# Optimization experiments

Hardware: AMD Instinct MI355X
Metric: run time of the kernel (lower is better)

The kernel has to match this reference:

```python
import jax, jax.numpy as jnp
import numpy as np

MULT = 0.001      # DEFAULT_MULTIPLIER
N_ITERS = 9       # self.N
N_K = 4           # self.l
BINARY = ('mul', 'add')  # original binary_ops_list order


def _valid_pairs(nc, r, lc):
    # replicate flag logic over (i, j) candidate pairs
    nri = N_ITERS - r
    out = []
    for i in range(nc - 1):
        for j in range(i + 1, nc):
            if nri == lc - 1:
                flag = i >= 3
            elif nri == lc:
                flag = j >= 3
            else:
                flag = nri > lc
            if flag:
                out.append((i, j))
    return out


def _act(name, res):
    if name == 'sigmoid':
        return MULT * jax.nn.sigmoid(res)
    if name == 'tanh':
        return MULT * jnp.tanh(res)
    if name == 'minus':
        return 1.0 - res
    return res  # identity


def run_cell(x, h_prev, L, R, b, w, plan=None):
    """Faithful RRNNforGRUCell tree-structure search.
    record mode (plan=None): data-dependent decisions taken concretely (eager).
    replay mode (plan given): purely differentiable jnp replay of recorded plan.
    """
    record = plan is None
    if record:
        plan = []
    xv = x.reshape(-1)
    hv = h_prev.reshape(-1)
    H = xv.shape[0]
    zero = jnp.zeros((H,), dtype=xv.dtype)
    G = []            # max_vector per iteration
    second = []       # second-ranked vector per iteration
    comp_src = []     # G-indices backing current components_list
    for r in range(N_ITERS):
        cand = [xv, hv, zero] + [G[g] for g in comp_src]
        nc = len(cand)
        C = jnp.stack(cand)                       # (nc, H)
        CL = jnp.einsum('ch,khd->ckd', C, L)      # (nc, 4, H) all s_i @ L_k
        CR = jnp.einsum('ch,khd->ckd', C, R)      # (nc, 4, H) all s_j @ R_k
        V = []
        if record:
            entries = []
            for (i, j) in _valid_pairs(nc, r, len(comp_src)):
                for k in range(N_K):
                    for bf in BINARY:
                        if bf == 'mul':
                            res = CL[i, k] * CR[j, k] + b[k]
                        else:
                            res = CL[i, k] + CR[j, k] + b[k]
                        if float(jnp.max(jnp.abs(res))) >= 1.0:
                            acts = ('sigmoid', 'tanh')
                        else:
                            acts = ('sigmoid', 'tanh', 'minus', 'identity')
                        for a in acts:
                            V.append(_act(a, res))
                            entries.append((i, j, k, bf, a))
        else:
            entries = plan[r]['entries']
            cache = {}
            for (i, j, k, bf, a) in entries:
                key = (i, j, k, bf)
                if key not in cache:
                    if bf == 'mul':
                        cache[key] = CL[i, k] * CR[j, k] + b[k]
                    else:
                        cache[key] = CL[i, k] + CR[j, k] + b[k]
                V.append(_act(a, cache[key]))
        Vs = jnp.stack(V)          # (nV, H)
        scores = Vs @ w            # (nV,) scoring Linear(H,1,bias=False)
        if record:
            s = np.asarray(scores)
            max_idx = int(np.argmax(s))
            # position of the element ranked second-smallest (original code)
            second_idx = int(np.where(np.argsort(s) == 1)[0][0])
            plan.append({'entries': entries, 'max_idx': max_idx, 'second_idx': second_idx})
        else:
            max_idx = plan[r]['max_idx']
            second_idx = plan[r]['second_idx']
        probs = jax.nn.softmax(scores)
        # NOTE: replicates original bug: loop uses stale `i` == nc-2, so every
        # v is weighted by probabilities[nc-2].
        max_vec = probs[nc - 2] * Vs.sum(axis=0)
        second.append(V[second_idx])
        G.append(max_vec)
        i, j = entries[max_idx][0], entries[max_idx][1]
        if i > 2 and j > 2:
            comp_src[i - 3] = r
            del comp_src[j - 3]
        elif i <= 2 and j > 2:
            comp_src[j - 3] = r
        else:
            comp_src.append(r)
    Gs = jnp.stack(G)                       # (9, H)
    out = (Gs[-1], Gs, Gs @ w, jnp.stack(second) @ w)
    return (out, plan) if record else out


def setup_inputs() -> dict:
    key = jax.random.key(0)
    ks = jax.random.split(key, 6)
    H = 2048
    return {
        'x': jax.random.normal(ks[0], (1, H), jnp.float32),
        'h_prev': jax.random.normal(ks[1], (1, H), jnp.float32),
        'L': MULT * jax.random.normal(ks[2], (N_K, H, H), jnp.float32),
        'R': MULT * jax.random.normal(ks[3], (N_K, H, H), jnp.float32),
        'b': MULT * jax.random.normal(ks[4], (N_K, H), jnp.float32),
        'w': jax.random.normal(ks[5], (H,), jnp.float32),
    }


def reference(x, h_prev, L, R, b, w):
    # returns (h_next, G_stack [9,H], scores of G [9], second_scores [9])
    out, _ = run_cell(x, h_prev, L, R, b, w)
    return out
```

## Files before the change

### kernel.cpp

```cpp
#include <hip/hip_runtime.h>
#include <math.h>

#define HDIM 2048
#define NK 4
#define NIT 9
#define NSID 11
#define MAXPAIRS 36
#define MAXBASES (MAXPAIRS*8)
#define NACC 16
#define NBS (MAXBASES + NACC)

#define CACHE_SZ (NSID*2*NK*HDIM)
#define OFF_CACHE 0
#define OFF_AMAX   (OFF_CACHE + CACHE_SZ)
#define OFF_DOTR_D (OFF_AMAX + MAXBASES)
#define OFF_DOTS_D (OFF_DOTR_D + 2*MAXBASES)
#define OFF_DOTT_D (OFF_DOTS_D + 2*MAXBASES)
#define PLAN_SZ 152
#define OFF_PLAN0 (OFF_DOTT_D + 2*MAXBASES)
#define OFF_PLAN1 (OFF_PLAN0 + PLAN_SZ)
#define OFF_STATE (OFF_PLAN1 + PLAN_SZ)
#define OFF_SUMW_D (OFF_STATE + 16)
#define OFF_GT8   (OFF_SUMW_D + 16)
#define OFF_PART  (OFF_GT8 + 8*HDIM)

__device__ __forceinline__ float wredmax(float v){
#pragma unroll
  for(int o=32;o;o>>=1) v = fmaxf(v,__shfl_down(v,o,64));
  return v;
}
__device__ __forceinline__ float wredsum(float v){
#pragma unroll
  for(int o=32;o;o>>=1) v += __shfl_down(v,o,64);
  return v;
}
__device__ __forceinline__ double wredsumd(double v){
#pragma unroll
  for(int o=32;o;o>>=1) v += __shfl_down(v,o,64);
  return v;
}

__device__ void build_plan(int r, int lc, const int* cs, int* plan){
  int nc = 3 + lc;
  int nri = NIT - r;
  int np = 0;
  for(int i=0;i<nc-1;i++){
    for(int j=i+1;j<nc;j++){
      bool flag;
      if (nri == lc-1)      flag = (i>=3);
      else if (nri == lc)   flag = (j>=3);
      else                  flag = (nri > lc);
      if(flag){
        plan[8+np]            = i;
        plan[8+MAXPAIRS+np]   = j;
        plan[8+2*MAXPAIRS+np] = (i<3)? i : 3+cs[i-3];
        plan[8+3*MAXPAIRS+np] = (j<3)? j : 3+cs[j-3];
        np++;
      }
    }
  }
  plan[0]=nc; plan[1]=np; plan[2]=np*8;
}

__global__ __launch_bounds__(256) void kvecmat(const float* __restrict__ va,
                                               const float* __restrict__ vb,
                                               const float* __restrict__ w,
                                               const float* __restrict__ L,
                                               const float* __restrict__ R,
                                               float* __restrict__ ws,
                                               int nvec){
  int bid = blockIdx.x;
  int tid = threadIdx.x;
  int nmain = nvec << 8;
  if (bid >= nmain){
    int ib = bid - nmain;
    for(int i = ib*256+tid; i < 8*HDIM; i += 32*256)
      ws[OFF_CACHE + 16*HDIM + i] = 0.f;
    if (ib == 0){
      double s = 0.0;
      for(int d=tid; d<HDIM; d+=256) s += (double)w[d];
      s = wredsumd(s);
      __shared__ double red[4];
      int wv = tid>>6, ln = tid&63;
      if(!ln) red[wv]=s;
      __syncthreads();
      if(tid==0){
        *(double*)(ws + OFF_SUMW_D) = red[0]+red[1]+red[2]+red[3];
        int* st = (int*)(ws + OFF_STATE);
        for(int q=0;q<=8;q++) st[q]=0;
        build_plan(0, 0, st+1, (int*)(ws + OFF_PLAN0));
      }
    }
    return;
  }
  int vec   = bid >> 8;
  int b     = bid & 255;
  int combo = b >> 5;
  int hc    = b & 31;
  const float* v = vec ? vb : va;
  __shared__ float vs[64];
  if (tid < 64) vs[tid] = v[hc*64 + tid];
  __syncthreads();
  int m = combo>>2, k = combo&3;
  const float* M = (m==0?L:R) + (size_t)k*HDIM*HDIM + (size_t)hc*64*HDIM + tid*4;
  float ax0=0.f, ay0=0.f, az0=0.f, aw0=0.f;
  float ax1=0.f, ay1=0.f, az1=0.f, aw1=0.f;
#pragma unroll 8
  for(int h=0; h<64; h++){
    const float4 f0 = *reinterpret_cast<const float4*>(M + (size_t)h*HDIM);
    const float4 f1 = *reinterpret_cast<const float4*>(M + (size_t)h*HDIM + 1024);
    float vv = vs[h];
    ax0 = fmaf(vv, f0.x, ax0); ay0 = fmaf(vv, f0.y, ay0);
    az0 = fmaf(vv, f0.z, az0); aw0 = fmaf(vv, f0.w, aw0);
    ax1 = fmaf(vv, f1.x, ax1); ay1 = fmaf(vv, f1.y, ay1);
    az1 = fmaf(vv, f1.z, az1); aw1 = fmaf(vv, f1.w, aw1);
  }
  float* P = ws + OFF_PART + ((size_t)(vec*8+combo)*32 + hc)*HDIM + tid*4;
  float4 o0; o0.x=ax0; o0.y=ay0; o0.z=az0; o0.w=aw0;
  float4 o1; o1.x=ax1; o1.y=ay1; o1.z=az1; o1.w=aw1;
  *reinterpret_cast<float4*>(P) = o0;
  *reinterpret_cast<float4*>(P + 1024) = o1;
}

__global__ __launch_bounds__(256) void kreduce(float* __restrict__ ws, int sid0){
  int b = blockIdx.x;
  int vec = b>>6, rem = b&63;
  int combo = rem>>3, dc8 = rem&7;
  int d = dc8*256 + threadIdx.x;
  const float* p = ws + OFF_PART + (size_t)(vec*8+combo)*32*HDIM + d;
  float s = 0.f;
#pragma unroll
  for(int hc=0; hc<32; hc++) s += p[(size_t)hc*HDIM];
  int m = combo>>2, k = combo&3;
  int sid = sid0 + vec;
  ws[OFF_CACHE + ((size_t)(sid*2+m)*NK + k)*HDIM + d] = s;
}

__global__ __launch_bounds__(256) void kbaseaccum(const float* __restrict__ bvec,
                                                  const float* __restrict__ w,
                                                  float* __restrict__ ws, int par){
  const int* plan = (const int*)(ws + (par ? OFF_PLAN1 : OFF_PLAN0));
  int nb = plan[2];
  int tid = threadIdx.x;
  if (blockIdx.x < MAXBASES){
    int t = blockIdx.x;
    if (t >= nb) return;
    int p = t>>3, k=(t>>1)&3, bf=t&1;
    int si = plan[8+2*MAXPAIRS+p], sj = plan[8+3*MAXPAIRS+p];
    const float* CL = ws + OFF_CACHE + ((size_t)(si*2+0)*NK + k)*HDIM;
    const float* CR = ws + OFF_CACHE + ((size_t)(sj*2+1)*NK + k)*HDIM;
    const float* bk = bvec + (size_t)k*HDIM;
    int d0 = tid*8;
    float am=0.f; double dr=0.0, ds=0.0, dt=0.0;
#pragma unroll
    for(int half=0; half<2; half++){
      int d = d0 + half*4;
      const float4 a4 = *reinterpret_cast<const float4*>(CL + d);
      const float4 c4 = *reinterpret_cast<const float4*>(CR + d);
      const float4 b4 = *reinterpret_cast<const float4*>(bk + d);
      const float4 w4 = *reinterpret_cast<const float4*>(w  + d);
      float av[4]={a4.x,a4.y,a4.z,a4.w};
      float cv[4]={c4.x,c4.y,c4.z,c4.w};
      float bv[4]={b4.x,b4.y,b4.z,b4.w};
      float wv4[4]={w4.x,w4.y,w4.z,w4.w};
#pragma unroll
      for(int q=0;q<4;q++){
        float res = (bf==0) ? __fadd_rn(__fmul_rn(av[q],cv[q]), bv[q])
                            : __fadd_rn(__fadd_rn(av[q],cv[q]), bv[q]);
        float wd = wv4[q];
        am = fmaxf(am, fabsf(res));
        float sg = 1.0f/(1.0f+expf(-res));
        float th = tanhf(res);
        dr += (double)res*(double)wd;
        ds += (double)sg *(double)wd;
        dt += (double)th *(double)wd;
      }
    }
    am = wredmax(am); dr = wredsumd(dr); ds = wredsumd(ds); dt = wredsumd(dt);
    __shared__ double redd[4][3];
    __shared__ float  redm[4];
    int wv = tid>>6, ln = tid&63;
    if(!ln){ redm[wv]=am; redd[wv][0]=dr; redd[wv][1]=ds; redd[wv][2]=dt; }
    __syncthreads();
    if(!tid){
      float A=redm[0]; double Dr=redd[0][0], Ds=redd[0][1], Dt=redd[0][2];
      for(int q=1;q<4;q++){ A=fmaxf(A,redm[q]); Dr+=redd[q][0]; Ds+=redd[q][1]; Dt+=redd[q][2]; }
      ws[OFF_AMAX+t]=A;
      ((double*)(ws+OFF_DOTR_D))[t]=Dr;
      ((double*)(ws+OFF_DOTS_D))[t]=Ds;
      ((double*)(ws+OFF_DOTT_D))[t]=Dt;
    }
  } else {
    int bid2 = blockIdx.x - MAXBASES;
    int bc = bid2 >> 1;
    int dh = bid2 & 1;
    int d = dh*1024 + tid*4;
    float acc[4] = {0.f,0.f,0.f,0.f};
    for(int t=bc; t<nb; t+=8){
      int p=t>>3, k=(t>>1)&3, bf=t&1;
      int si = plan[8+2*MAXPAIRS+p], sj = plan[8+3*MAXPAIRS+p];
      const float4 a4 = *reinterpret_cast<const float4*>(ws + OFF_CACHE + ((size_t)(si*2+0)*NK+k)*HDIM + d);
      const float4 c4 = *reinterpret_cast<const float4*>(ws + OFF_CACHE + ((size_t)(sj*2+1)*NK+k)*HDIM + d);
      const float4 b4 = *reinterpret_cast<const float4*>(bvec + (size_t)k*HDIM + d);
      float av[4]={a4.x,a4.y,a4.z,a4.w};
      float cv[4]={c4.x,c4.y,c4.z,c4.w};
      float bv[4]={b4.x,b4.y,b4.z,b4.w};
#pragma unroll
      for(int q=0;q<4;q++){
        float res = (bf==0) ? (av[q]*cv[q] + bv[q]) : (av[q] + cv[q] + bv[q]);
        float ex  = __expf(-res);
        float sig = 1.0f/(1.0f+ex);
        float ex2 = ex*ex;
        float th  = (1.0f-ex2)/(1.0f+ex2);
        acc[q] += sig + th;
      }
    }
    float4 o; o.x=acc[0]; o.y=acc[1]; o.z=acc[2]; o.w=acc[3];
    *reinterpret_cast<float4*>(ws + OFF_GT8 + (size_t)bc*HDIM + d) = o;
  }
}

__global__ __launch_bounds__(256) void kselfin(const float* __restrict__ w,
                                               float* __restrict__ ws,
                                               float* __restrict__ out, int r){
  __shared__ double s4[MAXBASES][4];
  __shared__ int    sna[MAXBASES];
  __shared__ double tval[256];
  __shared__ int    tidx[256];
  __shared__ double tz[256];
  __shared__ int    tcnt[256];
  __shared__ double sh_smax;
  __shared__ float  sh_psel;
  __shared__ int    sh_c4;
  int par = r & 1;
  int* plan = (int*)(ws + (par ? OFF_PLAN1 : OFF_PLAN0));
  int nc = plan[0];
  int nb = plan[2];
  double sumw = *(const double*)(ws + OFF_SUMW_D);
  const double* DR = (const double*)(ws+OFF_DOTR_D);
  const double* DS = (const double*)(ws+OFF_DOTS_D);
  const double* DT = (const double*)(ws+OFF_DOTT_D);
  int tid = threadIdx.x;
  for(int t=tid; t<nb; t+=256){
    float A  = ws[OFF_AMAX+t];
    double Dr = DR[t], Ds = DS[t], Dt = DT[t];
    sna[t] = (A < 1.0f) ? 4 : 2;
    s4[t][0] = 0.001*Ds;
    s4[t][1] = 0.001*Dt;
    s4[t][2] = sumw - Dr;
    s4[t][3] = Dr;
  }
  __syncthreads();
  double best = -1e300; int bidx = 1<<30;
  for(int q=tid; q<nb*4; q+=256){
    int t=q>>2, a=q&3;
    if (a < sna[t]){
      double v = s4[t][a];
      if (v > best || (v==best && q < bidx)){ best=v; bidx=q; }
    }
  }
  tval[tid]=best; tidx[tid]=bidx;
  __syncthreads();
  if (tid==0){
    double bb=tval[0]; int bi=tidx[0];
    for(int u=1;u<256;u++)
      if (tval[u] > bb || (tval[u]==bb && tidx[u] < bi)){ bb=tval[u]; bi=tidx[u]; }
    sh_smax = bb;
    tidx[0] = bi;
  }
  __syncthreads();
  double smax = sh_smax;
  double s1 = s4[0][1];
  double z = 0.0; int cnt = 0;
  for(int q=tid; q<nb*4; q+=256){
    int t=q>>2, a=q&3;
    if (a < sna[t]){
      double v = s4[t][a];
      z += exp(v - smax);
      cnt += (v < s1) ? 1 : 0;
    }
  }
  tz[tid]=z; tcnt[tid]=cnt;
  __syncthreads();
  if (tid==0){
    int bi = tidx[0];
    double Z=0.0; int rank=0;
    for(int u=0;u<256;u++){ Z += tz[u]; rank += tcnt[u]; }
    int need = nc-2, e=0; double s_sel=0.0;
    for(int t=0;t<nb;t++){
      int n = sna[t];
      if (need < e+n){ s_sel = s4[t][need-e]; break; }
      e += n;
    }
    double psel = exp(s_sel - smax) / Z;
    int e2=0; double ssec=0.0;
    for(int t=0;t<nb;t++){
      int n = sna[t];
      if (rank < e2+n){ ssec = s4[t][rank-e2]; break; }
      e2 += n;
    }
    out[10*HDIM + 9 + r] = (float)ssec;
    int c4=0;
    for(int t=0;t<nb;t++) c4 += (sna[t]==4) ? 1 : 0;
    int mt = bi>>2;
    int mp = mt>>3;
    int ci = plan[8+mp], cj = plan[8+MAXPAIRS+mp];
    sh_psel = (float)psel;
    sh_c4   = c4;
    int* st = (int*)(ws + OFF_STATE);
    int lc = st[0];
    int* cs = st+1;
    if (ci>2 && cj>2){
      cs[ci-3] = r;
      for(int q2=cj-3; q2<lc-1; q2++) cs[q2]=cs[q2+1];
      lc--;
    } else if (ci<=2 && cj>2){
      cs[cj-3] = r;
    } else {
      cs[lc] = r; lc++;
    }
    st[0]=lc;
    if (r+1 < NIT)
      build_plan(r+1, lc, cs, (int*)(ws + ((par^1) ? OFF_PLAN1 : OFF_PLAN0)));
  }
  __syncthreads();
  float psel = sh_psel;
  float c4f  = (float)sh_c4;
  float dot = 0.f;
#pragma unroll
  for(int q=0;q<8;q++){
    int d = q*256 + tid;
    float s = 0.f;
#pragma unroll
    for(int bc=0; bc<8; bc++) s += ws[OFF_GT8 + (size_t)bc*HDIM + d];
    float g = psel * (0.001f*s + c4f);
    out[HDIM + (size_t)r*HDIM + d] = g;
    if (r == NIT-1) out[d] = g;
    dot = fmaf(g, w[d], dot);
  }
  dot = wredsum(dot);
  __shared__ float redf[4];
  int wv = tid>>6, ln = tid&63;
  if(!ln) redf[wv]=dot;
  __syncthreads();
  if(!tid) out[10*HDIM + r] = redf[0]+redf[1]+redf[2]+redf[3];
}

extern "C" void kernel_launch(void* const* d_in, const int* in_sizes, int n_in,
                              void* d_out, int out_size, void* d_ws, size_t ws_size,
                              hipStream_t stream){
  const float* x = (const float*)d_in[0];
  const float* h = (const float*)d_in[1];
  const float* L = (const float*)d_in[2];
  const float* R = (const float*)d_in[3];
  const float* b = (const float*)d_in[4];
  const float* w = (const float*)d_in[5];
  float* out = (float*)d_out;
  float* ws  = (float*)d_ws;

  kvecmat<<<512+32,256,0,stream>>>(x, h, w, L, R, ws, 2);
  kreduce<<<128,256,0,stream>>>(ws, 0);
  for(int r=0;r<NIT;r++){
    if (r > 0){
      kvecmat<<<256,256,0,stream>>>(out + HDIM + (size_t)(r-1)*HDIM, nullptr, w, L, R, ws, 1);
      kreduce<<<64,256,0,stream>>>(ws, 3+(r-1));
    }
    kbaseaccum<<<NBS,256,0,stream>>>(b, w, ws, r&1);
    kselfin<<<1,256,0,stream>>>(w, ws, out, r);
  }
}
```

Measured before the change: 546.0 us.

## Stream matrix tiles through triple-buffered LDS with async global_load_lds

Replaces direct per-thread float4 global loads of the L/R tile rows with asynchronous global-to-LDS copies into a three-stage ring buffer. Explicit vmcnt waits and barriers let later tiles load while the current one is consumed from LDS. The aim is more bytes in flight and better overlap for this bandwidth-bound matrix-vector stage. The cost is 48KB of LDS per block, which may reduce occupancy, plus extra barriers and hand-tuned wait counts that must match the number of outstanding loads.

```diff
diff --git a/kernel.cpp b/kernel.cpp
--- a/kernel.cpp
+++ b/kernel.cpp
@@ -99,22 +99,52 @@
   int hc    = b & 31;
   const float* v = vec ? vb : va;
   __shared__ float vs[64];
+  __shared__ __align__(16) float lbuf[3][2*HDIM];
   if (tid < 64) vs[tid] = v[hc*64 + tid];
   __syncthreads();
   int m = combo>>2, k = combo&3;
-  const float* M = (m==0?L:R) + (size_t)k*HDIM*HDIM + (size_t)hc*64*HDIM + tid*4;
+  const float* tile = (m==0?L:R) + (size_t)k*HDIM*HDIM + (size_t)hc*64*HDIM;
+  int wv = tid >> 6, ln = tid & 63;
+
+#define STAGEC(g, bi) do{ \
+    const float* s_ = tile + (size_t)(g)*2*HDIM + (size_t)(wv*4)*256 + ln*4; \
+    _Pragma("unroll") \
+    for(int i_=0;i_<4;i_++){ \
+      __builtin_amdgcn_global_load_lds( \
+        (const __attribute__((address_space(1))) void*)(s_ + i_*256), \
+        (__attribute__((address_space(3))) void*)(&lbuf[bi][(wv*4+i_)*256]), \
+        16, 0, 0); \
+    } \
+  }while(0)
+
   float ax0=0.f, ay0=0.f, az0=0.f, aw0=0.f;
   float ax1=0.f, ay1=0.f, az1=0.f, aw1=0.f;
-#pragma unroll 8
-  for(int h=0; h<64; h++){
-    const float4 f0 = *reinterpret_cast<const float4*>(M + (size_t)h*HDIM);
-    const float4 f1 = *reinterpret_cast<const float4*>(M + (size_t)h*HDIM + 1024);
-    float vv = vs[h];
-    ax0 = fmaf(vv, f0.x, ax0); ay0 = fmaf(vv, f0.y, ay0);
-    az0 = fmaf(vv, f0.z, az0); aw0 = fmaf(vv, f0.w, aw0);
-    ax1 = fmaf(vv, f1.x, ax1); ay1 = fmaf(vv, f1.y, ay1);
-    az1 = fmaf(vv, f1.z, az1); aw1 = fmaf(vv, f1.w, aw1);
-  }
+  STAGEC(0,0);
+  STAGEC(1,1);
+  STAGEC(2,2);
+#pragma unroll
+  for(int g=0; g<32; g++){
+    int bi = g % 3;
+    if (g <= 29)      asm volatile("s_waitcnt vmcnt(8)" ::: "memory");
+    else if (g == 30) asm volatile("s_waitcnt vmcnt(4)" ::: "memory");
+    else              asm volatile("s_waitcnt vmcnt(0)" ::: "memory");
+    __builtin_amdgcn_s_barrier();
+    __builtin_amdgcn_sched_barrier(0);
+#pragma unroll
+    for(int rr=0; rr<2; rr++){
+      float vv = vs[g*2+rr];
+      const float4 f0 = *reinterpret_cast<const float4*>(&lbuf[bi][rr*HDIM + tid*4]);
+      const float4 f1 = *reinterpret_cast<const float4*>(&lbuf[bi][rr*HDIM + 1024 + tid*4]);
+      ax0 = fmaf(vv, f0.x, ax0); ay0 = fmaf(vv, f0.y, ay0);
+      az0 = fmaf(vv, f0.z, az0); aw0 = fmaf(vv, f0.w, aw0);
+      ax1 = fmaf(vv, f1.x, ax1); ay1 = fmaf(vv, f1.y, ay1);
+      az1 = fmaf(vv, f1.z, az1); aw1 = fmaf(vv, f1.w, aw1);
+    }
+    __builtin_amdgcn_sched_barrier(0);
+    __builtin_amdgcn_s_barrier();
+    if (g+3 < 32) STAGEC(g+3, bi);
+  }
+#undef STAGEC
   float* P = ws + OFF_PART + ((size_t)(vec*8+combo)*32 + hc)*HDIM + tid*4;
   float4 o0; o0.x=ax0; o0.y=ay0; o0.z=az0; o0.w=aw0;
   float4 o1; o1.x=ax1; o1.y=ay1; o1.z=az1; o1.w=aw1;
```

Measured after the change: 553.9 us. Within noise of the previous version (+1.4%).
